# Performance work log

Measured on AMD Instinct MI355X. Metric: run time of the kernel, lower is better.

Reference implementation:

```python
import jax, jax.numpy as jnp
import numpy as np
import math

D_MODEL = 1024
N_HEAD = 16
Q_DIM = K_DIM = V_DIM = 1024
SCALE = math.sqrt(D_MODEL // N_HEAD)  # 8.0
B, LQ, LK = 2, 2048, 2048


def setup_inputs() -> dict:
    key = jax.random.key(0)
    ks = jax.random.split(key, 10)
    s = 1.0 / math.sqrt(Q_DIM)
    return {
        "q": jax.random.normal(ks[0], (B, LQ, Q_DIM), jnp.float32),
        "k": jax.random.normal(ks[1], (B, LK, K_DIM), jnp.float32),
        "v": jax.random.normal(ks[2], (B, LK, V_DIM), jnp.float32),
        "mask": jax.random.randint(ks[3], (B, LQ, LK), 0, 2, jnp.int32),
        "Wq": jax.random.uniform(ks[4], (D_MODEL, Q_DIM), jnp.float32, -s, s),
        "bq": jnp.zeros((D_MODEL,), jnp.float32),
        "Wk": jax.random.uniform(ks[5], (D_MODEL, K_DIM), jnp.float32, -s, s),
        "bk": jnp.zeros((D_MODEL,), jnp.float32),
        "Wv": jax.random.uniform(ks[6], (D_MODEL, V_DIM), jnp.float32, -s, s),
        "bv": jnp.zeros((D_MODEL,), jnp.float32),
    }


def reference(q, k, v, Wq, bq, Wk, bk, Wv, bv, mask):
    b, lq, _ = q.shape
    lk = k.shape[1]
    dh = D_MODEL // N_HEAD
    # linear projections (torch Linear: x @ W.T + b)
    qh = (q @ Wq.T + bq).reshape(b, lq, N_HEAD, dh).transpose(0, 2, 1, 3)  # bhqd
    kh = (k @ Wk.T + bk).reshape(b, lk, N_HEAD, dh).transpose(0, 2, 1, 3)  # bhkd
    vh = (v @ Wv.T + bv).reshape(b, lk, N_HEAD, dh).transpose(0, 2, 1, 3)  # bhkd
    attn = jnp.einsum("bhqd,bhkd->bhqk", qh, kh) / SCALE
    m = mask[:, None, :, :]  # b1qk
    attn = jnp.where(m == 0, -jnp.inf, attn)
    # rows whose mask is all-zero are reset to 0 pre-softmax (-> uniform weights)
    row_empty = (m.sum(-1, keepdims=True) == 0)
    attn = jnp.where(row_empty, 0.0, attn)
    attn = jax.nn.softmax(attn, axis=-1)  # dropout is identity in eval mode
    v_out = jnp.einsum("bhqk,bhkd->bhqd", attn, vh)
    v_out = v_out.transpose(0, 2, 1, 3).reshape(b, lq, D_MODEL)
    k_out = jnp.einsum("bhqk,bhkd->bhqd", attn, kh)
    k_out = k_out.transpose(0, 2, 1, 3).reshape(b, lq, D_MODEL)
    return (k_out, v_out)
```

## Files before the change

kernel.cpp:

```cpp
#include <hip/hip_runtime.h>
#include <hip/hip_bf16.h>
#include <stdint.h>

typedef __bf16 bf16x8 __attribute__((ext_vector_type(8)));
typedef __bf16 bf16x4 __attribute__((ext_vector_type(4)));
typedef float f32x4 __attribute__((ext_vector_type(4)));

#define B_ 2
#define LQ_ 2048
#define LK_ 2048
#define NH_ 16
#define DH_ 64
#define DM_ 1024
#define NKT_ (LK_ / 64)

#define AS1 __attribute__((address_space(1)))
#define AS3 __attribute__((address_space(3)))

__device__ __forceinline__ void gload_lds16(const void* g, void* l) {
  __builtin_amdgcn_global_load_lds((const AS1 uint32_t*)g, (AS3 uint32_t*)l, 16, 0, 0);
}

__global__ __launch_bounds__(256) void prep_kernel(
    const float* __restrict__ q, const float* __restrict__ k,
    const float* __restrict__ v, const float* __restrict__ wq,
    const float* __restrict__ wk, const float* __restrict__ wv,
    const int* __restrict__ mask,
    __bf16* __restrict__ Xt0, __bf16* __restrict__ Xt1, __bf16* __restrict__ Xt2,
    __bf16* __restrict__ Wt0, __bf16* __restrict__ Wt1, __bf16* __restrict__ Wt2,
    unsigned* __restrict__ maskp) {
  const int t = threadIdx.x;
  const int bidx = blockIdx.x;
  if (bidx >= 960) {
    int pb = bidx - 960;
    int lane = t & 63;
    size_t gi = ((size_t)pb * 256 + t) * 4;
    int4 mv = *(const int4*)(mask + gi);
    unsigned nib = (mv.x != 0 ? 1u : 0u) | (mv.y != 0 ? 2u : 0u) |
                   (mv.z != 0 ? 4u : 0u) | (mv.w != 0 ? 8u : 0u);
    unsigned vv = nib << ((lane & 7) * 4);
    vv |= __shfl_xor(vv, 1, 64);
    vv |= __shfl_xor(vv, 2, 64);
    vv |= __shfl_xor(vv, 4, 64);
    if ((lane & 7) == 0) maskp[gi >> 5] = vv;
    return;
  }
  __shared__ __align__(16) __bf16 lb[16][1032];
  const float* src; __bf16* dst; int rows, m0;
  if (bidx < 256)      { src = q;  dst = Xt0; rows = 4096; m0 = bidx * 16; }
  else if (bidx < 512) { src = k;  dst = Xt1; rows = 4096; m0 = (bidx - 256) * 16; }
  else if (bidx < 768) { src = v;  dst = Xt2; rows = 4096; m0 = (bidx - 512) * 16; }
  else if (bidx < 832) { src = wq; dst = Wt0; rows = 1024; m0 = (bidx - 768) * 16; }
  else if (bidx < 896) { src = wk; dst = Wt1; rows = 1024; m0 = (bidx - 832) * 16; }
  else                 { src = wv; dst = Wt2; rows = 1024; m0 = (bidx - 896) * 16; }
#pragma unroll
  for (int i = 0; i < 16; i++) {
    float4 f = *(const float4*)(src + (size_t)(m0 + i) * DM_ + t * 4);
    bf16x4 o;
    o[0] = (__bf16)f.x; o[1] = (__bf16)f.y; o[2] = (__bf16)f.z; o[3] = (__bf16)f.w;
    *(bf16x4*)&lb[i][t * 4] = o;
  }
  __syncthreads();
  const int wave = t >> 6, lane = t & 63;
  const int m = lane >> 2, c = lane & 3;
#pragma unroll
  for (int j = 0; j < 8; j++) {
    int kt = wave * 8 + j;
    bf16x8 val = *(const bf16x8*)&lb[m][kt * 32 + (c ^ (m & 3)) * 8];
    *(bf16x8*)(dst + ((size_t)kt * rows + m0 + m) * 32 + c * 8) = val;
  }
}

__global__ __launch_bounds__(256) void proj_kernel(
    const __bf16* __restrict__ Xt0, const __bf16* __restrict__ Xt1,
    const __bf16* __restrict__ Xt2,
    const float* __restrict__ b0p, const float* __restrict__ b1p,
    const float* __restrict__ b2p,
    const __bf16* __restrict__ Wt0, const __bf16* __restrict__ Wt1,
    const __bf16* __restrict__ Wt2,
    __bf16* __restrict__ qh, __bf16* __restrict__ kh,
    __bf16* __restrict__ khT, __bf16* __restrict__ vhT) {
  __shared__ __align__(16) __bf16 smem[2][2][128 * 32];
  __bf16* cbuf = &smem[0][0][0];

  const int mode = blockIdx.z;
  const __bf16* Xt = mode == 0 ? Xt0 : (mode == 1 ? Xt1 : Xt2);
  const __bf16* Wt = mode == 0 ? Wt0 : (mode == 1 ? Wt1 : Wt2);
  const float* bias = mode == 0 ? b0p : (mode == 1 ? b1p : b2p);
  __bf16* ostd = mode == 0 ? qh : (mode == 1 ? kh : nullptr);
  __bf16* otr = mode == 0 ? nullptr : (mode == 1 ? khT : vhT);
  const float osc = mode == 0 ? 0.18033688f : 1.0f;

  const int t = threadIdx.x;
  const int wave = t >> 6, lane = t & 63;
  const int lo16 = lane & 15, quad = lane >> 4;
  const int wm = wave >> 1, wn = wave & 1;
  const int m0 = blockIdx.x * 128, n0 = blockIdx.y * 128;

  f32x4 acc[4][4] = {};

  auto stage = [&](int kt, int sel) {
#pragma unroll
    for (int ii = 2 * wave; ii < 2 * wave + 2; ii++) {
      gload_lds16(Xt + ((size_t)kt * 4096 + m0 + ii * 16) * 32 + lane * 8,
                  &smem[sel][0][ii * 512]);
      gload_lds16(Wt + ((size_t)kt * 1024 + n0 + ii * 16) * 32 + lane * 8,
                  &smem[sel][1][ii * 512]);
    }
  };

  stage(0, 0);
  for (int kt = 0; kt < 32; kt++) {
    const int sel = kt & 1;
    __syncthreads();
    if (kt + 1 < 32) stage(kt + 1, sel ^ 1);
    bf16x8 af[4], bfr[4];
#pragma unroll
    for (int g = 0; g < 4; g++) {
      int ar = wm * 64 + g * 16 + lo16;
      af[g] = *(const bf16x8*)(&smem[sel][0][ar * 32 + (quad ^ (ar & 3)) * 8]);
      int br = wn * 64 + g * 16 + lo16;
      bfr[g] = *(const bf16x8*)(&smem[sel][1][br * 32 + (quad ^ (br & 3)) * 8]);
    }
#pragma unroll
    for (int gm = 0; gm < 4; gm++)
#pragma unroll
      for (int gn = 0; gn < 4; gn++)
        acc[gm][gn] =
            __builtin_amdgcn_mfma_f32_16x16x32_bf16(af[gm], bfr[gn], acc[gm][gn], 0, 0, 0);
  }

  const int b = m0 >> 11, l0 = m0 & 2047;
  for (int nhf = 0; nhf < 2; nhf++) {
    int h = (n0 >> 6) + nhf;
    int bh = b * NH_ + h;
    if (ostd) {
      __syncthreads();
      if (wn == nhf) {
#pragma unroll
        for (int gn = 0; gn < 4; gn++) {
          float bi = bias[n0 + nhf * 64 + gn * 16 + lo16];
#pragma unroll
          for (int gm = 0; gm < 4; gm++)
#pragma unroll
            for (int r = 0; r < 4; r++)
              cbuf[(wm * 64 + gm * 16 + quad * 4 + r) * 72 + gn * 16 + lo16] =
                  (__bf16)((acc[gm][gn][r] + bi) * osc);
        }
      }
      __syncthreads();
      int m = t >> 1, coff = (t & 1) * 32;
      __bf16* dst = ostd + ((size_t)bh * LQ_ + l0 + m) * DH_ + coff;
#pragma unroll
      for (int j = 0; j < 4; j++)
        *(bf16x8*)(dst + j * 8) = *(const bf16x8*)&cbuf[m * 72 + coff + j * 8];
    }
    if (otr) {
      __syncthreads();
      if (wn == nhf) {
#pragma unroll
        for (int gn = 0; gn < 4; gn++) {
          float bi = bias[n0 + nhf * 64 + gn * 16 + lo16];
#pragma unroll
          for (int gm = 0; gm < 4; gm++) {
            bf16x4 pk;
#pragma unroll
            for (int r = 0; r < 4; r++) pk[r] = (__bf16)(acc[gm][gn][r] + bi);
            *(bf16x4*)&cbuf[(gn * 16 + lo16) * 136 + wm * 64 + gm * 16 + quad * 4] = pk;
          }
        }
      }
      __syncthreads();
      int d = t >> 2, mc = (t & 3) * 32;
      int kti = (l0 + mc) >> 6, kl = (l0 + mc) & 63;
      __bf16* dst = otr + ((size_t)(bh * NKT_ + kti) * 64 + d) * 64 + kl;
#pragma unroll
      for (int j = 0; j < 4; j++)
        *(bf16x8*)(dst + j * 8) = *(const bf16x8*)&cbuf[d * 136 + mc + j * 8];
    }
  }
}

__global__ __launch_bounds__(512) void attn_kernel(
    const __bf16* __restrict__ qh, const __bf16* __restrict__ kh,
    const __bf16* __restrict__ khT, const __bf16* __restrict__ vhT,
    const unsigned* __restrict__ maskp,
    float* __restrict__ out_k, float* __restrict__ out_v) {
  __shared__ __align__(16) __bf16 kbuf[2][64 * 64];
  __shared__ __align__(16) __bf16 ktbuf[2][64 * 64];
  __shared__ __align__(16) __bf16 vtbuf[2][64 * 64];
  __shared__ __align__(16) __bf16 p_lds[8][16][72];

  const int t = threadIdx.x;
  const int wave = t >> 6, lane = t & 63;
  const int lo16 = lane & 15, quad = lane >> 4;
  const int bh = blockIdx.x;
  const int b = bh >> 4, h = bh & 15;
  const int q0 = blockIdx.y * 128 + wave * 16;
  const int srow = lane >> 3;
  const int scg = (lane & 7) ^ srow;
  const int rsw = lo16 & 7;

  bf16x8 a_q0, a_q1;
  {
    const __bf16* qrow = qh + ((size_t)bh * LQ_ + q0 + lo16) * DH_ + quad * 8;
    a_q0 = *(const bf16x8*)(qrow);
    a_q1 = *(const bf16x8*)(qrow + 32);
  }

  bf16x8 ones;
#pragma unroll
  for (int j = 0; j < 8; j++) ones[j] = (__bf16)1.0f;

  f32x4 acc_v[4] = {};
  f32x4 acc_k[4] = {};
  f32x4 acc_l = {};

  const __bf16* khb = kh + (size_t)bh * LK_ * DH_;
  const __bf16* ktb = khT + (size_t)bh * LK_ * DH_;
  const __bf16* vtb = vhT + (size_t)bh * LK_ * DH_;

  const int row_s = wave * 8 + srow;
  auto stage = [&](int kti, int sel) {
    const int tb = kti * 4096;
    gload_lds16(khb + (size_t)(kti * 64 + row_s) * DH_ + scg * 8, &kbuf[sel][wave * 512]);
    gload_lds16(ktb + tb + row_s * 64 + scg * 8, &ktbuf[sel][wave * 512]);
    gload_lds16(vtb + tb + row_s * 64 + scg * 8, &vtbuf[sel][wave * 512]);
  };

  stage(0, 0);
  for (int kti = 0; kti < NKT_; kti++) {
    const int cur = kti & 1;
    __syncthreads();
    if (kti + 1 < NKT_) stage(kti + 1, cur ^ 1);

    const unsigned* mb =
        maskp + ((size_t)b * LQ_ + q0 + quad * 4) * (LK_ / 32) + kti * 2;
    unsigned mw0[4], mw1[4];
#pragma unroll
    for (int r = 0; r < 4; r++) {
      mw0[r] = mb[r * (LK_ / 32)];
      mw1[r] = mb[r * (LK_ / 32) + 1];
    }

    f32x4 s[4];
#pragma unroll
    for (int gg = 0; gg < 4; gg++) {
      int row = gg * 16 + lo16;
      bf16x8 kb0 = *(const bf16x8*)(&kbuf[cur][row * 64 + ((quad ^ rsw) * 8)]);
      bf16x8 kb1 = *(const bf16x8*)(&kbuf[cur][row * 64 + (((quad + 4) ^ rsw) * 8)]);
      f32x4 z = {};
      z = __builtin_amdgcn_mfma_f32_16x16x32_bf16(a_q0, kb0, z, 0, 0, 0);
      z = __builtin_amdgcn_mfma_f32_16x16x32_bf16(a_q1, kb1, z, 0, 0, 0);
      s[gg] = z;
    }

#pragma unroll
    for (int gg = 0; gg < 4; gg++) {
      int bitpos = (gg * 16 + lo16) & 31;
#pragma unroll
      for (int r = 0; r < 4; r++) {
        unsigned w = (gg >= 2) ? mw1[r] : mw0[r];
        float pe = __builtin_amdgcn_exp2f(s[gg][r]);
        s[gg][r] = ((w >> bitpos) & 1) ? pe : 0.0f;
      }
    }

#pragma unroll
    for (int gg = 0; gg < 4; gg++)
#pragma unroll
      for (int r = 0; r < 4; r++)
        p_lds[wave][quad * 4 + r][gg * 16 + lo16] = (__bf16)s[gg][r];
    bf16x8 a_p0 = *(const bf16x8*)&p_lds[wave][lo16][quad * 8];
    bf16x8 a_p1 = *(const bf16x8*)&p_lds[wave][lo16][32 + quad * 8];

#pragma unroll
    for (int gg = 0; gg < 4; gg++) {
      int row = gg * 16 + lo16;
      bf16x8 bv0 = *(const bf16x8*)(&vtbuf[cur][row * 64 + ((quad ^ rsw) * 8)]);
      bf16x8 bv1 = *(const bf16x8*)(&vtbuf[cur][row * 64 + (((quad + 4) ^ rsw) * 8)]);
      bf16x8 bk0 = *(const bf16x8*)(&ktbuf[cur][row * 64 + ((quad ^ rsw) * 8)]);
      bf16x8 bk1 = *(const bf16x8*)(&ktbuf[cur][row * 64 + (((quad + 4) ^ rsw) * 8)]);
      acc_v[gg] = __builtin_amdgcn_mfma_f32_16x16x32_bf16(a_p0, bv0, acc_v[gg], 0, 0, 0);
      acc_v[gg] = __builtin_amdgcn_mfma_f32_16x16x32_bf16(a_p1, bv1, acc_v[gg], 0, 0, 0);
      acc_k[gg] = __builtin_amdgcn_mfma_f32_16x16x32_bf16(a_p0, bk0, acc_k[gg], 0, 0, 0);
      acc_k[gg] = __builtin_amdgcn_mfma_f32_16x16x32_bf16(a_p1, bk1, acc_k[gg], 0, 0, 0);
    }
    acc_l = __builtin_amdgcn_mfma_f32_16x16x32_bf16(a_p0, ones, acc_l, 0, 0, 0);
    acc_l = __builtin_amdgcn_mfma_f32_16x16x32_bf16(a_p1, ones, acc_l, 0, 0, 0);
  }

  float inv_l[4];
#pragma unroll
  for (int r = 0; r < 4; r++) inv_l[r] = 1.0f / acc_l[r];
  size_t obase = ((size_t)b * LQ_ + q0 + quad * 4) * DM_ + h * DH_;
#pragma unroll
  for (int gg = 0; gg < 4; gg++) {
#pragma unroll
    for (int r = 0; r < 4; r++) {
      size_t idx = obase + (size_t)r * DM_ + gg * 16 + lo16;
      out_k[idx] = acc_k[gg][r] * inv_l[r];
      out_v[idx] = acc_v[gg][r] * inv_l[r];
    }
  }
}

extern "C" void kernel_launch(void* const* d_in, const int* in_sizes, int n_in,
                              void* d_out, int out_size, void* d_ws, size_t ws_size,
                              hipStream_t stream) {
  const float* q = (const float*)d_in[0];
  const float* k = (const float*)d_in[1];
  const float* v = (const float*)d_in[2];
  const int* mask = (const int*)d_in[3];
  const float* Wq = (const float*)d_in[4];
  const float* bq = (const float*)d_in[5];
  const float* Wk = (const float*)d_in[6];
  const float* bk = (const float*)d_in[7];
  const float* Wv = (const float*)d_in[8];
  const float* bv = (const float*)d_in[9];
  float* out = (float*)d_out;

  const size_t HTOT = (size_t)B_ * NH_ * LQ_ * DH_;
  const size_t XTOT = (size_t)B_ * LQ_ * DM_;
  __bf16* qh = (__bf16*)d_ws;
  __bf16* kh = qh + HTOT;
  __bf16* khT = kh + HTOT;
  __bf16* vhT = khT + HTOT;
  unsigned* maskp = (unsigned*)(vhT + HTOT);

  __bf16* Xt0 = (__bf16*)d_out;
  __bf16* Xt1 = Xt0 + XTOT;
  __bf16* Xt2 = Xt1 + XTOT;
  __bf16* Wt0 = Xt2 + XTOT;
  __bf16* Wt1 = Wt0 + (size_t)DM_ * DM_;
  __bf16* Wt2 = Wt1 + (size_t)DM_ * DM_;

  prep_kernel<<<960 + 8192, 256, 0, stream>>>(
      q, k, v, Wq, Wk, Wv, mask, Xt0, Xt1, Xt2, Wt0, Wt1, Wt2, maskp);
  proj_kernel<<<dim3(32, 8, 3), 256, 0, stream>>>(
      Xt0, Xt1, Xt2, bq, bk, bv, Wt0, Wt1, Wt2, qh, kh, khT, vhT);
  attn_kernel<<<dim3(32, 16), 512, 0, stream>>>(qh, kh, khT, vhT, maskp,
                                                out, out + (size_t)B_ * LQ_ * DM_);
}
```

Before: 263.8 us.

## Move mask packing into projection kernel and add MFMA priority hints

Mask bit-packing moves out of the prep kernel and into extra blocks (z=3) of the projection kernel, where each block handles 32 chunks. This lets the memory-bound mask read overlap with the compute-bound GEMM blocks. The attention kernel wraps its MFMA sections in s_setprio so those waves get issue priority. The bf16 scratch buffers move into the workspace when it is large enough, with the output buffer kept as a fallback.

```diff
diff --git a/kernel.cpp b/kernel.cpp
--- a/kernel.cpp
+++ b/kernel.cpp
@@ -25,26 +25,10 @@
     const float* __restrict__ q, const float* __restrict__ k,
     const float* __restrict__ v, const float* __restrict__ wq,
     const float* __restrict__ wk, const float* __restrict__ wv,
-    const int* __restrict__ mask,
     __bf16* __restrict__ Xt0, __bf16* __restrict__ Xt1, __bf16* __restrict__ Xt2,
-    __bf16* __restrict__ Wt0, __bf16* __restrict__ Wt1, __bf16* __restrict__ Wt2,
-    unsigned* __restrict__ maskp) {
+    __bf16* __restrict__ Wt0, __bf16* __restrict__ Wt1, __bf16* __restrict__ Wt2) {
   const int t = threadIdx.x;
   const int bidx = blockIdx.x;
-  if (bidx >= 960) {
-    int pb = bidx - 960;
-    int lane = t & 63;
-    size_t gi = ((size_t)pb * 256 + t) * 4;
-    int4 mv = *(const int4*)(mask + gi);
-    unsigned nib = (mv.x != 0 ? 1u : 0u) | (mv.y != 0 ? 2u : 0u) |
-                   (mv.z != 0 ? 4u : 0u) | (mv.w != 0 ? 8u : 0u);
-    unsigned vv = nib << ((lane & 7) * 4);
-    vv |= __shfl_xor(vv, 1, 64);
-    vv |= __shfl_xor(vv, 2, 64);
-    vv |= __shfl_xor(vv, 4, 64);
-    if ((lane & 7) == 0) maskp[gi >> 5] = vv;
-    return;
-  }
   __shared__ __align__(16) __bf16 lb[16][1032];
   const float* src; __bf16* dst; int rows, m0;
   if (bidx < 256)      { src = q;  dst = Xt0; rows = 4096; m0 = bidx * 16; }
@@ -79,11 +63,31 @@
     const __bf16* __restrict__ Wt0, const __bf16* __restrict__ Wt1,
     const __bf16* __restrict__ Wt2,
     __bf16* __restrict__ qh, __bf16* __restrict__ kh,
-    __bf16* __restrict__ khT, __bf16* __restrict__ vhT) {
+    __bf16* __restrict__ khT, __bf16* __restrict__ vhT,
+    const int* __restrict__ mask, unsigned* __restrict__ maskp) {
+  const int mode = blockIdx.z;
+  const int t = threadIdx.x;
+  if (mode == 3) {
+    int pb2 = blockIdx.x * 8 + blockIdx.y;
+    int lane = t & 63;
+#pragma unroll 4
+    for (int j = 0; j < 32; j++) {
+      int pb = pb2 + 256 * j;
+      size_t gi = ((size_t)pb * 256 + t) * 4;
+      int4 mv = *(const int4*)(mask + gi);
+      unsigned nib = (mv.x != 0 ? 1u : 0u) | (mv.y != 0 ? 2u : 0u) |
+                     (mv.z != 0 ? 4u : 0u) | (mv.w != 0 ? 8u : 0u);
+      unsigned vv = nib << ((lane & 7) * 4);
+      vv |= __shfl_xor(vv, 1, 64);
+      vv |= __shfl_xor(vv, 2, 64);
+      vv |= __shfl_xor(vv, 4, 64);
+      if ((lane & 7) == 0) maskp[gi >> 5] = vv;
+    }
+    return;
+  }
   __shared__ __align__(16) __bf16 smem[2][2][128 * 32];
   __bf16* cbuf = &smem[0][0][0];
 
-  const int mode = blockIdx.z;
   const __bf16* Xt = mode == 0 ? Xt0 : (mode == 1 ? Xt1 : Xt2);
   const __bf16* Wt = mode == 0 ? Wt0 : (mode == 1 ? Wt1 : Wt2);
   const float* bias = mode == 0 ? b0p : (mode == 1 ? b1p : b2p);
@@ -91,7 +95,6 @@
   __bf16* otr = mode == 0 ? nullptr : (mode == 1 ? khT : vhT);
   const float osc = mode == 0 ? 0.18033688f : 1.0f;
 
-  const int t = threadIdx.x;
   const int wave = t >> 6, lane = t & 63;
   const int lo16 = lane & 15, quad = lane >> 4;
   const int wm = wave >> 1, wn = wave & 1;
@@ -243,6 +246,7 @@
       mw1[r] = mb[r * (LK_ / 32) + 1];
     }
 
+    __builtin_amdgcn_s_setprio(1);
     f32x4 s[4];
 #pragma unroll
     for (int gg = 0; gg < 4; gg++) {
@@ -254,6 +258,7 @@
       z = __builtin_amdgcn_mfma_f32_16x16x32_bf16(a_q1, kb1, z, 0, 0, 0);
       s[gg] = z;
     }
+    __builtin_amdgcn_s_setprio(0);
 
 #pragma unroll
     for (int gg = 0; gg < 4; gg++) {
@@ -274,6 +279,7 @@
     bf16x8 a_p0 = *(const bf16x8*)&p_lds[wave][lo16][quad * 8];
     bf16x8 a_p1 = *(const bf16x8*)&p_lds[wave][lo16][32 + quad * 8];
 
+    __builtin_amdgcn_s_setprio(1);
 #pragma unroll
     for (int gg = 0; gg < 4; gg++) {
       int row = gg * 16 + lo16;
@@ -288,6 +294,7 @@
     }
     acc_l = __builtin_amdgcn_mfma_f32_16x16x32_bf16(a_p0, ones, acc_l, 0, 0, 0);
     acc_l = __builtin_amdgcn_mfma_f32_16x16x32_bf16(a_p1, ones, acc_l, 0, 0, 0);
+    __builtin_amdgcn_s_setprio(0);
   }
 
   float inv_l[4];
@@ -322,23 +329,28 @@
 
   const size_t HTOT = (size_t)B_ * NH_ * LQ_ * DH_;
   const size_t XTOT = (size_t)B_ * LQ_ * DM_;
+  const size_t MASKW = (size_t)B_ * LQ_ * (LK_ / 32);
   __bf16* qh = (__bf16*)d_ws;
   __bf16* kh = qh + HTOT;
   __bf16* khT = kh + HTOT;
   __bf16* vhT = khT + HTOT;
   unsigned* maskp = (unsigned*)(vhT + HTOT);
 
-  __bf16* Xt0 = (__bf16*)d_out;
+  const size_t SCR_ELEMS = 3 * XTOT + 3 * (size_t)DM_ * DM_;
+  const size_t NEED = 4 * HTOT * sizeof(__bf16) + MASKW * sizeof(unsigned) +
+                      SCR_ELEMS * sizeof(__bf16);
+  __bf16* scr = (ws_size >= NEED) ? (__bf16*)(maskp + MASKW) : (__bf16*)d_out;
+  __bf16* Xt0 = scr;
   __bf16* Xt1 = Xt0 + XTOT;
   __bf16* Xt2 = Xt1 + XTOT;
   __bf16* Wt0 = Xt2 + XTOT;
   __bf16* Wt1 = Wt0 + (size_t)DM_ * DM_;
   __bf16* Wt2 = Wt1 + (size_t)DM_ * DM_;
 
-  prep_kernel<<<960 + 8192, 256, 0, stream>>>(
-      q, k, v, Wq, Wk, Wv, mask, Xt0, Xt1, Xt2, Wt0, Wt1, Wt2, maskp);
-  proj_kernel<<<dim3(32, 8, 3), 256, 0, stream>>>(
-      Xt0, Xt1, Xt2, bq, bk, bv, Wt0, Wt1, Wt2, qh, kh, khT, vhT);
+  prep_kernel<<<960, 256, 0, stream>>>(
+      q, k, v, Wq, Wk, Wv, Xt0, Xt1, Xt2, Wt0, Wt1, Wt2);
+  proj_kernel<<<dim3(32, 8, 4), 256, 0, stream>>>(
+      Xt0, Xt1, Xt2, bq, bk, bv, Wt0, Wt1, Wt2, qh, kh, khT, vhT, mask, maskp);
   attn_kernel<<<dim3(32, 16), 512, 0, stream>>>(qh, kh, khT, vhT, maskp,
                                                 out, out + (size_t)B_ * LQ_ * DM_);
 }
```

Measured after the change: 263.8 us. About the same (-0.0%).

## Transpose QK^T MFMA output so P rows pack directly to LDS with one mask word

Applied to the files above, without the earlier changes.

Swaps the MFMA operands for the score tile so each lane holds four consecutive key columns of one query row. Each lane then reads just two mask words per tile instead of eight and writes P to LDS as packed bf16x4 vectors rather than scalar stores. Wave priority is also raised around the MFMA sections with s_setprio. Separately, the bf16 staging buffers move from the output buffer into workspace when the workspace is large enough.

```diff
diff --git a/kernel.cpp b/kernel.cpp
--- a/kernel.cpp
+++ b/kernel.cpp
@@ -235,14 +235,10 @@
     if (kti + 1 < NKT_) stage(kti + 1, cur ^ 1);
 
     const unsigned* mb =
-        maskp + ((size_t)b * LQ_ + q0 + quad * 4) * (LK_ / 32) + kti * 2;
-    unsigned mw0[4], mw1[4];
-#pragma unroll
-    for (int r = 0; r < 4; r++) {
-      mw0[r] = mb[r * (LK_ / 32)];
-      mw1[r] = mb[r * (LK_ / 32) + 1];
-    }
-
+        maskp + ((size_t)b * LQ_ + q0 + lo16) * (LK_ / 32) + kti * 2;
+    unsigned mw0 = mb[0], mw1 = mb[1];
+
+    __builtin_amdgcn_s_setprio(1);
     f32x4 s[4];
 #pragma unroll
     for (int gg = 0; gg < 4; gg++) {
@@ -250,30 +246,28 @@
       bf16x8 kb0 = *(const bf16x8*)(&kbuf[cur][row * 64 + ((quad ^ rsw) * 8)]);
       bf16x8 kb1 = *(const bf16x8*)(&kbuf[cur][row * 64 + (((quad + 4) ^ rsw) * 8)]);
       f32x4 z = {};
-      z = __builtin_amdgcn_mfma_f32_16x16x32_bf16(a_q0, kb0, z, 0, 0, 0);
-      z = __builtin_amdgcn_mfma_f32_16x16x32_bf16(a_q1, kb1, z, 0, 0, 0);
+      z = __builtin_amdgcn_mfma_f32_16x16x32_bf16(kb0, a_q0, z, 0, 0, 0);
+      z = __builtin_amdgcn_mfma_f32_16x16x32_bf16(kb1, a_q1, z, 0, 0, 0);
       s[gg] = z;
     }
+    __builtin_amdgcn_s_setprio(0);
 
 #pragma unroll
     for (int gg = 0; gg < 4; gg++) {
-      int bitpos = (gg * 16 + lo16) & 31;
+      unsigned w = (gg >= 2) ? mw1 : mw0;
+      bf16x4 pk;
 #pragma unroll
       for (int r = 0; r < 4; r++) {
-        unsigned w = (gg >= 2) ? mw1[r] : mw0[r];
+        int bitpos = (gg & 1) * 16 + quad * 4 + r;
         float pe = __builtin_amdgcn_exp2f(s[gg][r]);
-        s[gg][r] = ((w >> bitpos) & 1) ? pe : 0.0f;
+        pk[r] = ((w >> bitpos) & 1) ? (__bf16)pe : (__bf16)0.0f;
       }
-    }
-
-#pragma unroll
-    for (int gg = 0; gg < 4; gg++)
-#pragma unroll
-      for (int r = 0; r < 4; r++)
-        p_lds[wave][quad * 4 + r][gg * 16 + lo16] = (__bf16)s[gg][r];
+      *(bf16x4*)&p_lds[wave][lo16][gg * 16 + quad * 4] = pk;
+    }
     bf16x8 a_p0 = *(const bf16x8*)&p_lds[wave][lo16][quad * 8];
     bf16x8 a_p1 = *(const bf16x8*)&p_lds[wave][lo16][32 + quad * 8];
 
+    __builtin_amdgcn_s_setprio(1);
 #pragma unroll
     for (int gg = 0; gg < 4; gg++) {
       int row = gg * 16 + lo16;
@@ -288,6 +282,7 @@
     }
     acc_l = __builtin_amdgcn_mfma_f32_16x16x32_bf16(a_p0, ones, acc_l, 0, 0, 0);
     acc_l = __builtin_amdgcn_mfma_f32_16x16x32_bf16(a_p1, ones, acc_l, 0, 0, 0);
+    __builtin_amdgcn_s_setprio(0);
   }
 
   float inv_l[4];
@@ -322,13 +317,18 @@
 
   const size_t HTOT = (size_t)B_ * NH_ * LQ_ * DH_;
   const size_t XTOT = (size_t)B_ * LQ_ * DM_;
+  const size_t MASKW = (size_t)B_ * LQ_ * (LK_ / 32);
   __bf16* qh = (__bf16*)d_ws;
   __bf16* kh = qh + HTOT;
   __bf16* khT = kh + HTOT;
   __bf16* vhT = khT + HTOT;
   unsigned* maskp = (unsigned*)(vhT + HTOT);
 
-  __bf16* Xt0 = (__bf16*)d_out;
+  const size_t SCR_ELEMS = 3 * XTOT + 3 * (size_t)DM_ * DM_;
+  const size_t NEED = 4 * HTOT * sizeof(__bf16) + MASKW * sizeof(unsigned) +
+                      SCR_ELEMS * sizeof(__bf16);
+  __bf16* scr = (ws_size >= NEED) ? (__bf16*)(maskp + MASKW) : (__bf16*)d_out;
+  __bf16* Xt0 = scr;
   __bf16* Xt1 = Xt0 + XTOT;
   __bf16* Xt2 = Xt1 + XTOT;
   __bf16* Wt0 = Xt2 + XTOT;
```

Result: faster. 257.5 us (-2.4%).
